# Kernel optimization log

Hardware: AMD Instinct MI355X
Metric: run time of the kernel (lower is better)

The kernel has to match this reference:

```python
import jax, jax.numpy as jnp
import numpy as np

N = 50000   # nodes
E = 800000  # edges
D = 128     # input node features
H = 128     # hidden channels
G = 250     # graphs in batch
EPS = 1e-5  # BatchNorm eps


def _lin(k, fi, fo):
    s = 1.0 / np.sqrt(fi)
    return jax.random.uniform(k, (fi, fo), jnp.float32, -s, s)


def setup_inputs() -> dict:
    key = jax.random.key(0)
    ks = jax.random.split(key, 16)
    x = jax.random.normal(ks[0], (N, D), jnp.float32)
    edge_index = jax.random.randint(ks[1], (2, E), 0, N)
    batch = jnp.sort(jax.random.randint(ks[2], (N,), 0, G))
    return {
        "x": x, "edge_index": edge_index, "batch": batch,
        "W1": _lin(ks[3], D, H), "b1": jnp.zeros((H,), jnp.float32),
        "g1": jnp.ones((H,), jnp.float32), "be1": jnp.zeros((H,), jnp.float32),
        "W2": _lin(ks[4], H, H), "b2": jnp.zeros((H,), jnp.float32),
        "g2": jnp.ones((H,), jnp.float32), "be2": jnp.zeros((H,), jnp.float32),
        "W3": _lin(ks[5], H, H), "b3": jnp.zeros((H,), jnp.float32),
        "g3": jnp.ones((H,), jnp.float32), "be3": jnp.zeros((H,), jnp.float32),
        "Wm1": _lin(ks[6], H, H), "bm1": _lin(ks[7], H, 1)[:, 0],
        "Wm2": _lin(ks[8], H, 1), "bm2": _lin(ks[9], 1, 1)[:, 0],
    }


def gcn_conv(x, W, b, src, dst, n):
    # PyG GCNConv: h = x W; add self-loops; symmetric deg^{-1/2} normalization;
    # scatter-add messages from src to dst; add bias.
    h = x @ W                                     # [N, H]
    deg = jnp.zeros((n,), h.dtype).at[dst].add(1.0) + 1.0  # in-degree + self-loop
    dis = deg ** -0.5
    coef = dis[src] * dis[dst]                    # [E]
    agg = jax.ops.segment_sum(h[src] * coef[:, None], dst, num_segments=n)
    return agg + h * (1.0 / deg)[:, None] + b     # self-loop term: norm = 1/deg


def bn_relu(x, g, be):
    # BatchNorm1d training-mode stats (biased variance), then ReLU
    m = jnp.mean(x, axis=0)
    v = jnp.mean((x - m) ** 2, axis=0)
    return jax.nn.relu((x - m) * jax.lax.rsqrt(v + EPS) * g + be)


def reference(x, edge_index, batch, W1, b1, g1, be1, W2, b2, g2, be2,
              W3, b3, g3, be3, Wm1, bm1, Wm2, bm2):
    src, dst = edge_index[0], edge_index[1]
    h = bn_relu(gcn_conv(x, W1, b1, src, dst, N), g1, be1)
    h = bn_relu(gcn_conv(h, W2, b2, src, dst, N), g2, be2)
    h = bn_relu(gcn_conv(h, W3, b3, src, dst, N), g3, be3)
    p = jax.ops.segment_sum(h, batch, num_segments=G)   # global_add_pool -> [G, H]
    p = jax.nn.relu(p @ Wm1 + bm1)                      # dropout is identity (eval)
    return p @ Wm2 + bm2                                # [G, 1]
```

## Files before the change

kernel.cpp:

```cpp
#include <hip/hip_runtime.h>

#define NN 50000
#define NE 800000
#define DD 128
#define NG 250
#define BN_EPS 1e-5f
#define ELLW 64
#define GATHER_BLOCKS 2048
#define NSLOT 32

typedef unsigned short u16;
typedef __attribute__((ext_vector_type(8))) short bf16x8;
typedef __attribute__((ext_vector_type(4))) float f32x4;

__device__ inline u16 f2bf(float f) {
    union { float f; unsigned u; } c;
    c.f = f;
    unsigned r = c.u + 0x7fffu + ((c.u >> 16) & 1u);
    return (u16)(r >> 16);
}
__device__ inline float bf2f(u16 h) {
    union { unsigned u; float f; } c;
    c.u = (unsigned)h << 16;
    return c.f;
}
__device__ inline unsigned pack2bf(float lo, float hi) {
    return (unsigned)f2bf(lo) | ((unsigned)f2bf(hi) << 16);
}
__device__ inline float bf_lo(unsigned u) {
    union { unsigned u; float f; } c;
    c.u = u << 16;
    return c.f;
}
__device__ inline float bf_hi(unsigned u) {
    union { unsigned u; float f; } c;
    c.u = u & 0xffff0000u;
    return c.f;
}


__global__ void fillell_k(const int* __restrict__ src, const int* __restrict__ dst,
                          int* __restrict__ fc, u16* __restrict__ ell) {
    int e = blockIdx.x * 256 + threadIdx.x;
    if (e < NE) {
        int d = dst[e];
        int pos = atomicAdd(&fc[d], 1);
        if (pos < ELLW) ell[(size_t)d * ELLW + pos] = (u16)src[e];
    }
}

__global__ void dis_k(const int* __restrict__ fc, float* __restrict__ dis) {
    int i = blockIdx.x * 256 + threadIdx.x;
    if (i < NN) dis[i] = 1.0f / sqrtf((float)(fc[i] + 1));
}


__global__ void wprep_k(const float* __restrict__ W1, const float* __restrict__ W2,
                        const float* __restrict__ W3, u16* __restrict__ wt) {
    int lid = blockIdx.x >> 6;
    int idx = (blockIdx.x & 63) * 256 + threadIdx.x;
    const float* W = lid == 0 ? W1 : (lid == 1 ? W2 : W3);
    int k = idx >> 7, n = idx & 127;
    float w = W[idx];
    u16 hi = f2bf(w);
    u16 lo = f2bf(w - bf2f(hi));
    wt[((size_t)lid * 2 + 0) * 16384 + (size_t)n * 128 + k] = hi;
    wt[((size_t)lid * 2 + 1) * 16384 + (size_t)n * 128 + k] = lo;
}


__global__ __launch_bounds__(256) void mgemm_k(const float* __restrict__ A32,
                                               const u16* __restrict__ A16,
                                               const u16* __restrict__ WT,
                                               const float* __restrict__ sc,
                                               const float* __restrict__ sh,
                                               const float* __restrict__ dis,
                                               u16* __restrict__ HB, int use_bn) {
    __shared__ u16 WL[2 * 128 * 128];
    __shared__ float scs[128], shs[128];
    int tid = threadIdx.x;
    if (use_bn && tid < 128) { scs[tid] = sc[tid]; shs[tid] = sh[tid]; }
    {
        const uint4* wg = (const uint4*)WT;
#pragma unroll
        for (int i = 0; i < 16; i++) {
            int ci = tid + i * 256;
            unsigned byte = (unsigned)ci * 16;
            unsigned n = (byte >> 8) & 127;
            unsigned swz = byte ^ ((n & 7) << 4);
            *(uint4*)((char*)WL + swz) = wg[ci];
        }
    }
    __syncthreads();

    int w = tid >> 6, lane = tid & 63;
    int col = lane & 15, lg = lane >> 4;
    int rowA = blockIdx.x * 64 + w * 16 + col;

    union { uint4 q; bf16x8 v; } afr[4];
#pragma unroll
    for (int s = 0; s < 4; s++) afr[s].q = make_uint4(0, 0, 0, 0);
    if (rowA < NN) {
        if (!use_bn) {
            const float4* ap = (const float4*)(A32 + (size_t)rowA * DD);
#pragma unroll
            for (int s = 0; s < 4; s++) {
                float4 f0 = ap[s * 8 + lg * 2];
                float4 f1 = ap[s * 8 + lg * 2 + 1];
                afr[s].q = make_uint4(pack2bf(f0.x, f0.y), pack2bf(f0.z, f0.w),
                                      pack2bf(f1.x, f1.y), pack2bf(f1.z, f1.w));
            }
        } else {
            const uint4* ap = (const uint4*)(A16 + (size_t)rowA * DD);
#pragma unroll
            for (int s = 0; s < 4; s++) {
                uint4 q = ap[s * 4 + lg];
                unsigned uu[4] = {q.x, q.y, q.z, q.w};
                int cbase = s * 32 + lg * 8;
#pragma unroll
                for (int t = 0; t < 4; t++) {
                    int c0 = cbase + t * 2;
                    float f0 = fmaxf(fmaf(bf_lo(uu[t]), scs[c0], shs[c0]), 0.f);
                    float f1 = fmaxf(fmaf(bf_hi(uu[t]), scs[c0 + 1], shs[c0 + 1]), 0.f);
                    uu[t] = pack2bf(f0, f1);
                }
                afr[s].q = make_uint4(uu[0], uu[1], uu[2], uu[3]);
            }
        }
    }

    f32x4 acc[8];
#pragma unroll
    for (int cf = 0; cf < 8; cf++) { acc[cf][0] = 0.f; acc[cf][1] = 0.f; acc[cf][2] = 0.f; acc[cf][3] = 0.f; }

#pragma unroll
    for (int half = 0; half < 2; half++) {
#pragma unroll
        for (int s = 0; s < 4; s++) {
#pragma unroll
            for (int cf = 0; cf < 8; cf++) {
                int nn = cf * 16 + col;
                unsigned byte = (unsigned)half * 32768 + (unsigned)nn * 256
                              + (unsigned)(s * 64 + lg * 16);
                byte ^= ((nn & 7) << 4);
                bf16x8 b = *(const bf16x8*)((const char*)WL + byte);
                acc[cf] = __builtin_amdgcn_mfma_f32_16x16x32_bf16(afr[s].v, b, acc[cf], 0, 0, 0);
            }
        }
    }

#pragma unroll
    for (int r = 0; r < 4; r++) {
        int ro = blockIdx.x * 64 + w * 16 + lg * 4 + r;
        if (ro < NN) {
            float dv = dis[ro];
#pragma unroll
            for (int cf = 0; cf < 8; cf++) {
                HB[(size_t)ro * DD + cf * 16 + col] = f2bf(acc[cf][r] * dv);
            }
        }
    }
}


__global__ __launch_bounds__(256) void gather_k(const u16* __restrict__ HB,
                                                const float* __restrict__ dis,
                                                const int* __restrict__ fc,
                                                const u16* __restrict__ ell,
                                                const float* __restrict__ bias,
                                                u16* __restrict__ AGG,
                                                float* __restrict__ statsP) {
    __shared__ float s_sum[128], s_sq[128];
    int tid = threadIdx.x;
    if (tid < 128) { s_sum[tid] = 0.f; s_sq[tid] = 0.f; }
    __syncthreads();
    int lane = tid & 63;
    int wid = blockIdx.x * 4 + (tid >> 6);
    const int nwaves = GATHER_BLOCKS * 4;
    int c = lane * 2;
    float b0 = bias[c], b1 = bias[c + 1];
    float lsum0 = 0.f, lsum1 = 0.f, lsq0 = 0.f, lsq1 = 0.f;
    for (int v = wid; v < NN; v += nwaves) {
        int cntv = fc[v];
        if (cntv > ELLW) cntv = ELLW;
        int myidx = (lane < cntv) ? (int)ell[(size_t)v * ELLW + lane] : 0;
        float a0 = 0.f, a1 = 0.f;
        int j = 0;
        for (; j + 8 <= cntv; j += 8) {
            unsigned r[8];
#pragma unroll
            for (int q = 0; q < 8; q++) {
                int s = __shfl(myidx, j + q);
                r[q] = *(const unsigned*)(HB + (size_t)s * DD + c);
            }
#pragma unroll
            for (int q = 0; q < 8; q++) { a0 += bf_lo(r[q]); a1 += bf_hi(r[q]); }
        }
        for (; j < cntv; j++) {
            int s = __shfl(myidx, j);
            unsigned r0 = *(const unsigned*)(HB + (size_t)s * DD + c);
            a0 += bf_lo(r0);
            a1 += bf_hi(r0);
        }
        unsigned rsf = *(const unsigned*)(HB + (size_t)v * DD + c);
        float dv = dis[v];
        float o0 = fmaf(a0 + bf_lo(rsf), dv, b0);
        float o1 = fmaf(a1 + bf_hi(rsf), dv, b1);
        *(unsigned*)(AGG + (size_t)v * DD + c) = pack2bf(o0, o1);
        lsum0 += o0; lsum1 += o1;
        lsq0 += o0 * o0; lsq1 += o1 * o1;
    }
    atomicAdd(&s_sum[c], lsum0);
    atomicAdd(&s_sum[c + 1], lsum1);
    atomicAdd(&s_sq[c], lsq0);
    atomicAdd(&s_sq[c + 1], lsq1);
    __syncthreads();
    if (tid < 128) {
        float* slot = statsP + (size_t)(blockIdx.x & (NSLOT - 1)) * 256;
        atomicAdd(&slot[tid], s_sum[tid]);
        atomicAdd(&slot[128 + tid], s_sq[tid]);
    }
}


__global__ void bnfix_k(const float* __restrict__ statsP, const float* __restrict__ g,
                        const float* __restrict__ be, float* __restrict__ sc,
                        float* __restrict__ sh) {
    int c = threadIdx.x;
    float sum = 0.f, sq = 0.f;
#pragma unroll
    for (int s = 0; s < NSLOT; s++) {
        sum += statsP[(size_t)s * 256 + c];
        sq  += statsP[(size_t)s * 256 + 128 + c];
    }
    float mean = sum * (1.0f / NN);
    float var = sq * (1.0f / NN) - mean * mean;
    float scl = g[c] / sqrtf(var + BN_EPS);
    sc[c] = scl;
    sh[c] = be[c] - mean * scl;
}


__global__ __launch_bounds__(256) void pool_k(const u16* __restrict__ AGG,
                                              const int* __restrict__ batch,
                                              const float* __restrict__ sc,
                                              const float* __restrict__ sh,
                                              float* __restrict__ P) {
    int lane = threadIdx.x & 63;
    int wid = blockIdx.x * 4 + (threadIdx.x >> 6);
    int nw = gridDim.x * 4;
    int c = lane * 2;
    float sc0 = sc[c], sc1 = sc[c + 1], sh0 = sh[c], sh1 = sh[c + 1];
    int chunk = (NN + nw - 1) / nw;
    int v0 = wid * chunk, v1 = v0 + chunk;
    if (v1 > NN) v1 = NN;
    if (v0 >= NN) return;
    int curb = batch[v0];
    float acc0 = 0.f, acc1 = 0.f;
    for (int v = v0; v < v1; v++) {
        int b = batch[v];
        if (b != curb) {
            atomicAdd(&P[curb * 128 + c], acc0);
            atomicAdd(&P[curb * 128 + c + 1], acc1);
            acc0 = 0.f; acc1 = 0.f; curb = b;
        }
        unsigned hv = *(const unsigned*)(AGG + (size_t)v * DD + c);
        acc0 += fmaxf(fmaf(bf_lo(hv), sc0, sh0), 0.f);
        acc1 += fmaxf(fmaf(bf_hi(hv), sc1, sh1), 0.f);
    }
    atomicAdd(&P[curb * 128 + c], acc0);
    atomicAdd(&P[curb * 128 + c + 1], acc1);
}


__global__ __launch_bounds__(128) void head_k(const float* __restrict__ P,
                                              const float* __restrict__ Wm1,
                                              const float* __restrict__ bm1,
                                              const float* __restrict__ Wm2,
                                              const float* __restrict__ bm2,
                                              float* __restrict__ OUT) {
    __shared__ float prow[128];
    __shared__ float red[128];
    int g = blockIdx.x, t = threadIdx.x;
    prow[t] = P[g * 128 + t];
    __syncthreads();
    float acc = bm1[t];
#pragma unroll 8
    for (int i = 0; i < 128; i++) acc = fmaf(prow[i], Wm1[i * 128 + t], acc);
    red[t] = fmaxf(acc, 0.f) * Wm2[t];
    __syncthreads();
    for (int off = 64; off > 0; off >>= 1) {
        if (t < off) red[t] += red[t + off];
        __syncthreads();
    }
    if (t == 0) OUT[g] = red[0] + bm2[0];
}


extern "C" void kernel_launch(void* const* d_in, const int* in_sizes, int n_in,
                              void* d_out, int out_size, void* d_ws, size_t ws_size,
                              hipStream_t stream) {
    const float* x   = (const float*)d_in[0];
    const int*  ei   = (const int*)d_in[1];
    const int*  batch= (const int*)d_in[2];
    const float* W1  = (const float*)d_in[3];
    const float* b1  = (const float*)d_in[4];
    const float* g1  = (const float*)d_in[5];
    const float* be1 = (const float*)d_in[6];
    const float* W2  = (const float*)d_in[7];
    const float* b2  = (const float*)d_in[8];
    const float* g2  = (const float*)d_in[9];
    const float* be2 = (const float*)d_in[10];
    const float* W3  = (const float*)d_in[11];
    const float* b3  = (const float*)d_in[12];
    const float* g3  = (const float*)d_in[13];
    const float* be3 = (const float*)d_in[14];
    const float* Wm1 = (const float*)d_in[15];
    const float* bm1 = (const float*)d_in[16];
    const float* Wm2 = (const float*)d_in[17];
    const float* bm2 = (const float*)d_in[18];
    float* out = (float*)d_out;

    char* ws = (char*)d_ws;
    size_t off = 0;
    auto alloc = [&](size_t bytes) -> void* {
        void* p = ws + off;
        off = (off + bytes + 255) & ~(size_t)255;
        return p;
    };
    int*   fc    = (int*)alloc((size_t)NN * 4);
    float* dis   = (float*)alloc((size_t)NN * 4);
    u16*   ell   = (u16*)alloc((size_t)NN * ELLW * 2);
    u16*   hb    = (u16*)alloc((size_t)NN * DD * 2);
    u16*   agg   = (u16*)alloc((size_t)NN * DD * 2);
    u16*   wt    = (u16*)alloc((size_t)3 * 2 * 16384 * 2);
    float* statsP= (float*)alloc((size_t)3 * NSLOT * 256 * 4);
    float* scb   = (float*)alloc(3 * 128 * 4);
    float* shb   = (float*)alloc(3 * 128 * 4);
    float* p     = (float*)alloc((size_t)NG * DD * 4);

    const int* srcI = ei;
    const int* dstI = ei + NE;

    hipMemsetAsync(fc, 0, (size_t)NN * 4, stream);
    hipMemsetAsync(statsP, 0, (size_t)3 * NSLOT * 256 * 4, stream);
    hipMemsetAsync(p, 0, (size_t)NG * DD * 4, stream);

    fillell_k<<<(NE + 255) / 256, 256, 0, stream>>>(srcI, dstI, fc, ell);
    dis_k<<<(NN + 255) / 256, 256, 0, stream>>>(fc, dis);
    wprep_k<<<192, 256, 0, stream>>>(W1, W2, W3, wt);

    const int GB = (NN + 63) / 64;
    const size_t SL = (size_t)NSLOT * 256;

    mgemm_k<<<GB, 256, 0, stream>>>(x, nullptr, wt, nullptr, nullptr, dis, hb, 0);
    gather_k<<<GATHER_BLOCKS, 256, 0, stream>>>(hb, dis, fc, ell, b1, agg, statsP);
    bnfix_k<<<1, 128, 0, stream>>>(statsP, g1, be1, scb, shb);

    mgemm_k<<<GB, 256, 0, stream>>>(nullptr, agg, wt + 2 * 16384, scb, shb, dis, hb, 1);
    gather_k<<<GATHER_BLOCKS, 256, 0, stream>>>(hb, dis, fc, ell, b2, agg, statsP + SL);
    bnfix_k<<<1, 128, 0, stream>>>(statsP + SL, g2, be2, scb + 128, shb + 128);

    mgemm_k<<<GB, 256, 0, stream>>>(nullptr, agg, wt + 4 * 16384, scb + 128, shb + 128, dis, hb, 1);
    gather_k<<<GATHER_BLOCKS, 256, 0, stream>>>(hb, dis, fc, ell, b3, agg, statsP + 2 * SL);
    bnfix_k<<<1, 128, 0, stream>>>(statsP + 2 * SL, g3, be3, scb + 256, shb + 256);

    pool_k<<<512, 256, 0, stream>>>(agg, batch, scb + 256, shb + 256, p);
    head_k<<<NG, 128, 0, stream>>>(p, Wm1, bm1, Wm2, bm2, out);
}
```

Measured before the change: 354.8 us.

## Build ELL adjacency via two-pass shared-memory bucketing instead of global atomics

Replaces the per-edge global-atomic ELL fill with two passes. The first bins edges by destination range into LDS and flushes them to global buckets. The second builds each bucket's ELL rows in LDS and writes them out coalesced, computing degree and normalisation in the same pass. The BN stats slot count is raised and three memsets are merged into one. The aim is to cut global atomic contention and scattered 2-byte writes, at the cost of an extra bucket buffer and fixed capacity limits (BKCAP) that could drop edges on skewed graphs.

```diff
diff --git a/kernel.cpp b/kernel.cpp
--- a/kernel.cpp
+++ b/kernel.cpp
@@ -7,7 +7,13 @@
 #define BN_EPS 1e-5f
 #define ELLW 64
 #define GATHER_BLOCKS 2048
-#define NSLOT 32
+#define NSLOT 128
+
+#define NBK 256
+#define BKRANGE 196
+#define BKCAP 4608
+#define P1_BLOCKS 250
+#define P1_CHUNK 3200
 
 typedef unsigned short u16;
 typedef __attribute__((ext_vector_type(8))) short bf16x8;
@@ -39,19 +45,82 @@
 }
 
 
-__global__ void fillell_k(const int* __restrict__ src, const int* __restrict__ dst,
-                          int* __restrict__ fc, u16* __restrict__ ell) {
-    int e = blockIdx.x * 256 + threadIdx.x;
-    if (e < NE) {
-        int d = dst[e];
-        int pos = atomicAdd(&fc[d], 1);
-        if (pos < ELLW) ell[(size_t)d * ELLW + pos] = (u16)src[e];
-    }
-}
-
-__global__ void dis_k(const int* __restrict__ fc, float* __restrict__ dis) {
-    int i = blockIdx.x * 256 + threadIdx.x;
-    if (i < NN) dis[i] = 1.0f / sqrtf((float)(fc[i] + 1));
+__global__ __launch_bounds__(256) void binpass_k(const int* __restrict__ src,
+                                                 const int* __restrict__ dst,
+                                                 int* __restrict__ bcnt,
+                                                 unsigned* __restrict__ buckets) {
+    __shared__ unsigned bins[NBK][64];
+    __shared__ int bn[NBK];
+    __shared__ int bbase[NBK];
+    int tid = threadIdx.x;
+    for (int i = tid; i < NBK; i += 256) bn[i] = 0;
+    __syncthreads();
+    int e0 = blockIdx.x * P1_CHUNK;
+    for (int i = tid; i < P1_CHUNK; i += 256) {
+        int e = e0 + i;
+        if (e < NE) {
+            int d = dst[e];
+            int s = src[e];
+            int bk = d / BKRANGE;
+            int dl = d - bk * BKRANGE;
+            unsigned ent = ((unsigned)dl << 16) | (unsigned)s;
+            int pos = atomicAdd(&bn[bk], 1);
+            if (pos < 64) {
+                bins[bk][pos] = ent;
+            } else {
+                int gb = atomicAdd(&bcnt[bk], 1);
+                if (gb < BKCAP) buckets[(size_t)bk * BKCAP + gb] = ent;
+            }
+        }
+    }
+    __syncthreads();
+    if (tid < NBK) {
+        int cnt = bn[tid]; if (cnt > 64) cnt = 64;
+        bbase[tid] = cnt ? atomicAdd(&bcnt[tid], cnt) : 0;
+    }
+    __syncthreads();
+    if (tid < NBK) {
+        int cnt = bn[tid]; if (cnt > 64) cnt = 64;
+        int base = bbase[tid];
+        unsigned* gb = buckets + (size_t)tid * BKCAP;
+        for (int i = 0; i < cnt; i++) {
+            int g = base + i;
+            if (g < BKCAP) gb[g] = bins[tid][i];
+        }
+    }
+}
+
+
+__global__ __launch_bounds__(256) void ellpass_k(const int* __restrict__ bcnt,
+                                                 const unsigned* __restrict__ buckets,
+                                                 int* __restrict__ fc,
+                                                 float* __restrict__ dis,
+                                                 u16* __restrict__ ell) {
+    __shared__ u16 lell[BKRANGE * ELLW];
+    __shared__ int lcnt[BKRANGE];
+    int b = blockIdx.x, tid = threadIdx.x;
+    for (int i = tid; i < BKRANGE; i += 256) lcnt[i] = 0;
+    __syncthreads();
+    int cnt = bcnt[b]; if (cnt > BKCAP) cnt = BKCAP;
+    const unsigned* bk = buckets + (size_t)b * BKCAP;
+    for (int i = tid; i < cnt; i += 256) {
+        unsigned ent = bk[i];
+        int dl = ent >> 16;
+        int pos = atomicAdd(&lcnt[dl], 1);
+        if (pos < ELLW) lell[dl * ELLW + pos] = (u16)(ent & 0xffffu);
+    }
+    __syncthreads();
+    int n0 = b * BKRANGE;
+    int nrows = NN - n0; if (nrows > BKRANGE) nrows = BKRANGE; if (nrows < 0) nrows = 0;
+    int words = nrows * (ELLW / 2);
+    unsigned* gell = (unsigned*)(ell + (size_t)n0 * ELLW);
+    const unsigned* l32 = (const unsigned*)lell;
+    for (int i = tid; i < words; i += 256) gell[i] = l32[i];
+    for (int i = tid; i < nrows; i += 256) {
+        int c = lcnt[i]; if (c > ELLW) c = ELLW;
+        fc[n0 + i] = c;
+        dis[n0 + i] = 1.0f / sqrtf((float)(c + 1));
+    }
 }
 
 
@@ -228,7 +297,6 @@
                         float* __restrict__ sh) {
     int c = threadIdx.x;
     float sum = 0.f, sq = 0.f;
-#pragma unroll
     for (int s = 0; s < NSLOT; s++) {
         sum += statsP[(size_t)s * 256 + c];
         sq  += statsP[(size_t)s * 256 + 128 + c];
@@ -334,20 +402,20 @@
     u16*   hb    = (u16*)alloc((size_t)NN * DD * 2);
     u16*   agg   = (u16*)alloc((size_t)NN * DD * 2);
     u16*   wt    = (u16*)alloc((size_t)3 * 2 * 16384 * 2);
-    float* statsP= (float*)alloc((size_t)3 * NSLOT * 256 * 4);
     float* scb   = (float*)alloc(3 * 128 * 4);
     float* shb   = (float*)alloc(3 * 128 * 4);
+    unsigned* buckets = (unsigned*)alloc((size_t)NBK * BKCAP * 4);
+    float* statsP= (float*)alloc((size_t)3 * NSLOT * 256 * 4);
     float* p     = (float*)alloc((size_t)NG * DD * 4);
+    int*   bcnt  = (int*)alloc((size_t)NBK * 4);
 
     const int* srcI = ei;
     const int* dstI = ei + NE;
 
-    hipMemsetAsync(fc, 0, (size_t)NN * 4, stream);
-    hipMemsetAsync(statsP, 0, (size_t)3 * NSLOT * 256 * 4, stream);
-    hipMemsetAsync(p, 0, (size_t)NG * DD * 4, stream);
-
-    fillell_k<<<(NE + 255) / 256, 256, 0, stream>>>(srcI, dstI, fc, ell);
-    dis_k<<<(NN + 255) / 256, 256, 0, stream>>>(fc, dis);
+    hipMemsetAsync(statsP, 0, (size_t)3 * NSLOT * 256 * 4 + (size_t)NG * DD * 4 + (size_t)NBK * 4, stream);
+
+    binpass_k<<<P1_BLOCKS, 256, 0, stream>>>(srcI, dstI, bcnt, buckets);
+    ellpass_k<<<NBK, 256, 0, stream>>>(bcnt, buckets, fc, dis, ell);
     wprep_k<<<192, 256, 0, stream>>>(W1, W2, W3, wt);
 
     const int GB = (NN + 63) / 64;
```

After: 333.5 us. 1.06x faster.
